# Performance work log

Measured on AMD Instinct MI355X. Metric: run time of the kernel, lower is better.

The kernel has to match this reference:

```python
import jax, jax.numpy as jnp
import numpy as np

B, K, L, C = 8192, 8, 1000, 100000  # batch, layers, labels, calibration size


def setup_inputs() -> dict:
    key = jax.random.key(0)
    k1, k2, k3 = jax.random.split(key, 3)
    nonconformity = jax.random.normal(k1, (B, K, L), dtype=jnp.float32)
    label_sample = jax.random.randint(k2, (L,), 0, L, dtype=jnp.int64 if jax.config.jax_enable_x64 else jnp.int32)
    cali_nonconformity = jax.random.normal(k3, (C,), dtype=jnp.float32)
    return {
        "nonconformity": nonconformity,
        "label_sample": label_sample,
        "cali_nonconformity": cali_nonconformity,
    }


def reference(nonconformity, label_sample, cali_nonconformity):
    # label_sample only defines the number of labels (axis 2 of nonconformity).
    cali_num = cali_nonconformity.shape[0]
    # Sum per-layer nonconformity over layers: [B, K, L] -> [B, L]
    total = jnp.sum(nonconformity, axis=1)
    # Empirical p-value: fraction of calibration scores >= total.
    # count(cali >= s) = C - (# of cali strictly < s) via sorted searchsorted.
    sorted_cali = jnp.sort(cali_nonconformity)
    num_less = jnp.searchsorted(sorted_cali, total, side="left")  # [B, L] ints
    p_value = (cali_num - num_less).astype(jnp.float32) / cali_num
    return p_value
```

## Files before the change

### kernel.cpp

```cpp
#include <hip/hip_runtime.h>


#define NBINS 8192
#define BIN_LO 8.0f
#define BIN_SCALE 512.0f
#define BLOCK 1024

typedef float floatx4 __attribute__((ext_vector_type(4)));

__device__ __forceinline__ int bin_of(float c) {
    float t = (c + BIN_LO) * BIN_SCALE;
    t = fminf(t, (float)(NBINS - 1));
    t = fmaxf(t, 0.0f);
    return (int)t;
}

__device__ __forceinline__ void scan_pval(int* tbl, int* wsum, int C, float invC) {
    const int t = threadIdx.x;
    const int lane = t & 63;
    const int wid = t >> 6;
    const int base = t * 8;
    float* ftbl = (float*)tbl;
    int h[8];
    int sum = 0;
    #pragma unroll
    for (int i = 0; i < 8; ++i) { h[i] = tbl[base + i]; sum += h[i]; }
    int inc = sum;
    #pragma unroll
    for (int off = 1; off < 64; off <<= 1) {
        int v = __shfl_up(inc, off);
        if (lane >= off) inc += v;
    }
    if (lane == 63) wsum[wid] = inc;
    __syncthreads();
    if (wid == 0) {
        int w = (lane < 16) ? wsum[lane] : 0;
        int winc = w;
        #pragma unroll
        for (int off = 1; off < 16; off <<= 1) {
            int v = __shfl_up(winc, off);
            if (lane >= off) winc += v;
        }
        if (lane < 16) wsum[lane] = winc - w;
    }
    __syncthreads();
    int run = wsum[wid] + (inc - sum);
    #pragma unroll
    for (int i = 0; i < 8; ++i) {
        int midc = (2 * run + h[i]) >> 1;
        ftbl[base + i] = (float)(C - midc) * invC;
        run += h[i];
    }
}

struct Buf { float4 v[8]; };

__device__ __forceinline__ void load8(Buf& bf, const float* __restrict__ p, int L) {
    #pragma unroll
    for (int k = 0; k < 8; ++k)
        bf.v[k] = *reinterpret_cast<const float4*>(p + k * L);
}

__device__ __forceinline__ void fold8(const Buf& bf, float s[4]) {
    s[0] = ((bf.v[0].x + bf.v[1].x) + (bf.v[2].x + bf.v[3].x)) +
           ((bf.v[4].x + bf.v[5].x) + (bf.v[6].x + bf.v[7].x));
    s[1] = ((bf.v[0].y + bf.v[1].y) + (bf.v[2].y + bf.v[3].y)) +
           ((bf.v[4].y + bf.v[5].y) + (bf.v[6].y + bf.v[7].y));
    s[2] = ((bf.v[0].z + bf.v[1].z) + (bf.v[2].z + bf.v[3].z)) +
           ((bf.v[4].z + bf.v[5].z) + (bf.v[6].z + bf.v[7].z));
    s[3] = ((bf.v[0].w + bf.v[1].w) + (bf.v[2].w + bf.v[3].w)) +
           ((bf.v[4].w + bf.v[5].w) + (bf.v[6].w + bf.v[7].w));
}

__device__ __forceinline__ void lookup_store_nt(const float* ftbl, const float s[4],
                                                float* __restrict__ out, int idx) {
    floatx4 p;
    p.x = ftbl[bin_of(s[0])];
    p.y = ftbl[bin_of(s[1])];
    p.z = ftbl[bin_of(s[2])];
    p.w = ftbl[bin_of(s[3])];
    __builtin_nontemporal_store(p, reinterpret_cast<floatx4*>(out + (idx << 2)));
}

template <int LT>
__global__ __launch_bounds__(BLOCK, 4) void dknn_k8_pipent_kernel(
        const float* __restrict__ nc, const float* __restrict__ cali,
        float* __restrict__ out, int n4, int Lrt, int C, float invC) {
    const int L = (LT > 0) ? LT : Lrt;
    const int L7 = 7 * L;
    __shared__ int tbl[NBINS];
    __shared__ int wsum[16];
    const float* ftbl = (const float*)tbl;
    const int t = threadIdx.x;
    const int gid = blockIdx.x * BLOCK + t;
    const int nth = gridDim.x * BLOCK;

    auto rb = [&](int idx) -> const float* {
        int flat = idx << 2;
        int b = flat / L;
        return nc + (size_t)((unsigned)flat + (unsigned)b * (unsigned)L7);
    };

    int iA = gid;
    int iB = gid + nth;
    Buf A, B;
    load8(A, rb(min(iA, n4 - 1)), L);
    load8(B, rb(min(iB, n4 - 1)), L);
    __builtin_amdgcn_sched_barrier(0);

    #pragma unroll
    for (int i = 0; i < NBINS / BLOCK; ++i) tbl[t + i * BLOCK] = 0;
    __syncthreads();

    {
        const int nvec = C >> 2;
        const float4* cali4 = (const float4*)cali;
        for (int i = t; i < nvec; i += BLOCK) {
            float4 v = cali4[i];
            atomicAdd(&tbl[bin_of(v.x)], 1);
            atomicAdd(&tbl[bin_of(v.y)], 1);
            atomicAdd(&tbl[bin_of(v.z)], 1);
            atomicAdd(&tbl[bin_of(v.w)], 1);
        }
        for (int i = (nvec << 2) + t; i < C; i += BLOCK)
            atomicAdd(&tbl[bin_of(cali[i])], 1);
    }

    __syncthreads();
    scan_pval(tbl, wsum, C, invC);
    __syncthreads();

    while (iA < n4) {
        float s[4];
        fold8(A, s);
        lookup_store_nt(ftbl, s, out, iA);
        int iN = iB + nth;
        load8(A, rb(min(iN, n4 - 1)), L);
        if (iB < n4) {
            float r[4];
            fold8(B, r);
            lookup_store_nt(ftbl, r, out, iB);
        }
        int iM = iN + nth;
        load8(B, rb(min(iM, n4 - 1)), L);
        iA = iN;
        iB = iM;
    }
}

__global__ __launch_bounds__(BLOCK, 4) void dknn_generic_kernel(
        const float* __restrict__ nc, const float* __restrict__ cali,
        float* __restrict__ out, int BL, int K, int L, int C, float invC) {
    __shared__ int tbl[NBINS];
    __shared__ int wsum[16];
    const float* ftbl = (const float*)tbl;
    const int t = threadIdx.x;
    #pragma unroll
    for (int i = 0; i < NBINS / BLOCK; ++i) tbl[t + i * BLOCK] = 0;
    __syncthreads();
    for (int i = t; i < C; i += BLOCK) atomicAdd(&tbl[bin_of(cali[i])], 1);
    __syncthreads();
    scan_pval(tbl, wsum, C, invC);
    __syncthreads();
    const int stride = gridDim.x * BLOCK;
    for (int i = blockIdx.x * BLOCK + t; i < BL; i += stride) {
        int b = i / L;
        int l = i - b * L;
        const float* base = nc + (size_t)b * (size_t)K * (size_t)L + l;
        float s = 0.f;
        for (int k = 0; k < K; ++k) s += base[(size_t)k * L];
        out[i] = ftbl[bin_of(s)];
    }
}

extern "C" void kernel_launch(void* const* d_in, const int* in_sizes, int n_in,
                              void* d_out, int out_size, void* d_ws, size_t ws_size,
                              hipStream_t stream) {
    const float* nc   = (const float*)d_in[0];
    const float* cali = (const float*)d_in[2];

    const int L  = in_sizes[1];
    const int C  = in_sizes[2];
    const int BL = out_size;
    const int K  = in_sizes[0] / BL;
    const float invC = 1.0f / (float)C;
    float* out = (float*)d_out;

    if ((L & 3) == 0 && K == 8 && BL >= 4) {
        int n4 = BL >> 2;
        int nblocks = 256;
        int needed = (n4 + BLOCK - 1) / BLOCK;
        if (nblocks > needed) nblocks = needed;
        if (L == 1000) {
            dknn_k8_pipent_kernel<1000><<<nblocks, BLOCK, 0, stream>>>(
                nc, cali, out, n4, L, C, invC);
        } else {
            dknn_k8_pipent_kernel<0><<<nblocks, BLOCK, 0, stream>>>(
                nc, cali, out, n4, L, C, invC);
        }
    } else {
        int nblocks = 512;
        int needed = (BL + BLOCK - 1) / BLOCK;
        if (nblocks > needed) nblocks = needed;
        dknn_generic_kernel<<<nblocks, BLOCK, 0, stream>>>(
            nc, cali, out, BL, K, L, C, invC);
    }
}
```

Before: 57.54 us.

## Warp-specialize histogram build and overlap it with input streaming

Splits each block into 256 histogram threads and 768 streaming threads, so the calibration histogram is built while other warps load and reduce nonconformity rows into register buffers. Work is partitioned into contiguous per-block chunks instead of a grid stride. This hides the per-block histogram latency behind memory traffic, at the cost of a slower histogram with fewer threads and more registers for the buffered sums, which risks spills.

Measured after the change: 83.19 us. 44.6% more time.

```diff
diff --git a/kernel.cpp b/kernel.cpp
--- a/kernel.cpp
+++ b/kernel.cpp
@@ -5,6 +5,9 @@
 #define BIN_LO 8.0f
 #define BIN_SCALE 512.0f
 #define BLOCK 1024
+#define HISTT 256
+#define NSTR (BLOCK - HISTT)
+#define NBUF 6
 
 typedef float floatx4 __attribute__((ext_vector_type(4)));
 
@@ -83,7 +86,7 @@
 }
 
 template <int LT>
-__global__ __launch_bounds__(BLOCK, 4) void dknn_k8_pipent_kernel(
+__global__ __launch_bounds__(BLOCK, 4) void dknn_k8_ws_kernel(
         const float* __restrict__ nc, const float* __restrict__ cali,
         float* __restrict__ out, int n4, int Lrt, int C, float invC) {
     const int L = (LT > 0) ? LT : Lrt;
@@ -92,8 +95,10 @@
     __shared__ int wsum[16];
     const float* ftbl = (const float*)tbl;
     const int t = threadIdx.x;
-    const int gid = blockIdx.x * BLOCK + t;
-    const int nth = gridDim.x * BLOCK;
+
+    const int W = (n4 + gridDim.x - 1) / gridDim.x;
+    const int beg = blockIdx.x * W;
+    const int end = min(n4, beg + W);
 
     auto rb = [&](int idx) -> const float* {
         int flat = idx << 2;
@@ -101,50 +106,69 @@
         return nc + (size_t)((unsigned)flat + (unsigned)b * (unsigned)L7);
     };
 
-    int iA = gid;
-    int iB = gid + nth;
+    #pragma unroll
+    for (int i = 0; i < NBINS / BLOCK; ++i) tbl[t + i * BLOCK] = 0;
+    __syncthreads();
+
     Buf A, B;
-    load8(A, rb(min(iA, n4 - 1)), L);
-    load8(B, rb(min(iB, n4 - 1)), L);
-    __builtin_amdgcn_sched_barrier(0);
-
-    #pragma unroll
-    for (int i = 0; i < NBINS / BLOCK; ++i) tbl[t + i * BLOCK] = 0;
-    __syncthreads();
-
-    {
+    float sums[NBUF][4];
+    const int st = t - HISTT;
+    const int i0 = beg + st;
+
+    if (t < HISTT) {
         const int nvec = C >> 2;
         const float4* cali4 = (const float4*)cali;
-        for (int i = t; i < nvec; i += BLOCK) {
+        for (int i = t; i < nvec; i += HISTT) {
             float4 v = cali4[i];
             atomicAdd(&tbl[bin_of(v.x)], 1);
             atomicAdd(&tbl[bin_of(v.y)], 1);
             atomicAdd(&tbl[bin_of(v.z)], 1);
             atomicAdd(&tbl[bin_of(v.w)], 1);
         }
-        for (int i = (nvec << 2) + t; i < C; i += BLOCK)
+        for (int i = (nvec << 2) + t; i < C; i += HISTT)
             atomicAdd(&tbl[bin_of(cali[i])], 1);
-    }
-
+    } else {
+        load8(A, rb(min(i0, n4 - 1)), L);
+        load8(B, rb(min(i0 + NSTR, n4 - 1)), L);
+        #pragma unroll
+        for (int j = 0; j < NBUF; ++j) {
+            if (j & 1) {
+                fold8(B, sums[j]);
+                load8(B, rb(min(i0 + (j + 2) * NSTR, n4 - 1)), L);
+            } else {
+                fold8(A, sums[j]);
+                load8(A, rb(min(i0 + (j + 2) * NSTR, n4 - 1)), L);
+            }
+        }
+    }
     __syncthreads();
     scan_pval(tbl, wsum, C, invC);
     __syncthreads();
 
-    while (iA < n4) {
-        float s[4];
-        fold8(A, s);
-        lookup_store_nt(ftbl, s, out, iA);
-        int iN = iB + nth;
-        load8(A, rb(min(iN, n4 - 1)), L);
-        if (iB < n4) {
-            float r[4];
-            fold8(B, r);
-            lookup_store_nt(ftbl, r, out, iB);
-        }
-        int iM = iN + nth;
-        load8(B, rb(min(iM, n4 - 1)), L);
-        iA = iN;
-        iB = iM;
+    if (t >= HISTT) {
+        #pragma unroll
+        for (int j = 0; j < NBUF; ++j) {
+            int idx = i0 + j * NSTR;
+            if (idx < end) lookup_store_nt(ftbl, sums[j], out, idx);
+        }
+        int iA = i0 + NBUF * NSTR;
+        int iB = iA + NSTR;
+        while (iA < end) {
+            float s[4];
+            fold8(A, s);
+            lookup_store_nt(ftbl, s, out, iA);
+            int iN = iB + NSTR;
+            load8(A, rb(min(iN, n4 - 1)), L);
+            if (iB < end) {
+                float r[4];
+                fold8(B, r);
+                lookup_store_nt(ftbl, r, out, iB);
+            }
+            int iM = iN + NSTR;
+            load8(B, rb(min(iM, n4 - 1)), L);
+            iA = iN;
+            iB = iM;
+        }
     }
 }
 
@@ -192,10 +216,10 @@
         int needed = (n4 + BLOCK - 1) / BLOCK;
         if (nblocks > needed) nblocks = needed;
         if (L == 1000) {
-            dknn_k8_pipent_kernel<1000><<<nblocks, BLOCK, 0, stream>>>(
+            dknn_k8_ws_kernel<1000><<<nblocks, BLOCK, 0, stream>>>(
                 nc, cali, out, n4, L, C, invC);
         } else {
-            dknn_k8_pipent_kernel<0><<<nblocks, BLOCK, 0, stream>>>(
+            dknn_k8_ws_kernel<0><<<nblocks, BLOCK, 0, stream>>>(
                 nc, cali, out, n4, L, C, invC);
         }
     } else {
```
